# Kernel optimization log

Hardware: AMD Instinct MI355X
Metric: run time of the kernel (lower is better)

Reference implementation:

```python
import jax, jax.numpy as jnp
import numpy as np

BITS = 4            # OPU.bits
VEC = 64            # OPU.input_vector_len / weight_vector_len
QMAX = 2 ** (BITS - 1) - 1   # 7


def ste_round(x):
    # straight-through round (onn_round)
    return x + jax.lax.stop_gradient(jnp.round(x) - x)


@jax.custom_vjp
def onn_dot_sum(x, w):
    # x: [N, R, VEC], w: [VEC, R, M]
    # per-chunk matmul -> clamp to int8 range -> binarize (>=0 -> 1) -> sum over chunks
    s = jnp.einsum('nrc,crm->nrm', x, w)
    s = jnp.clip(s, -128.0, 127.0)
    return jnp.where(s < 0, 0.0, 1.0).sum(axis=1)  # [N, M]


def _onn_dot_fwd(x, w):
    return onn_dot_sum(x, w), (x, w)


def _onn_dot_bwd(res, g):
    # onn_dot_fun.backward: straight-through past clamp+threshold;
    # each chunk receives the same grad g (sum over chunks).
    x, w = res
    gx = jnp.einsum('nm,crm->nrc', g, w)
    gw = jnp.einsum('nrc,nm->crm', x, g)
    return gx, gw


onn_dot_sum.defvjp(_onn_dot_fwd, _onn_dot_bwd)


def _onn_conv2d(inp, weight):
    B, C, H, W = inp.shape
    Cout, Cin, k, _ = weight.shape
    pad = (k - 1) // 2  # SAME, stride=1
    # im2col (matches torch F.unfold channel-major ordering: C, kh, kw)
    xp = jnp.pad(inp, ((0, 0), (0, 0), (pad, pad), (pad, pad)))
    patches = jnp.stack([xp[:, :, i:i + H, j:j + W]
                         for i in range(k) for j in range(k)], axis=2)  # [B,C,k*k,H,W]
    inp_unf = patches.reshape(B, C * k * k, H * W).transpose(0, 2, 1)    # [B,L,D]
    # weight quantization: STE round + clamp to 4-bit signed range
    scale = (2 ** BITS - 1) / (weight.max() - weight.min() + 1e-9)
    wq = jnp.clip(ste_round(weight * scale), -QMAX, QMAX)
    w_ = wq.reshape(Cout, -1).T                                          # [D, Cout]
    D = C * k * k
    repeats = -(-D // VEC)
    padD = VEC * repeats - D
    x = jnp.pad(inp_unf, ((0, 0), (0, 0), (0, padD))).reshape(B * H * W, repeats, VEC)
    wpad = jnp.pad(w_, ((0, padD), (0, 0)))                              # [VEC*R, Cout]
    wr = wpad.T.reshape(Cout, repeats, VEC).transpose(2, 1, 0)           # [VEC,R,Cout]
    temp = onn_dot_sum(x, wr)                                            # [B*L, Cout]
    return temp.reshape(B, H * W, Cout).transpose(0, 2, 1).reshape(B, Cout, H, W)


def setup_inputs() -> dict:
    key = jax.random.key(0)
    k1, k2 = jax.random.split(key)
    B, Cin, H, W = 16, 128, 32, 32
    Cout, k = 256, 3
    inp = jax.random.normal(k1, (B, Cin, H, W), dtype=jnp.float32)
    fan_in = Cin * k * k
    bound = 1.0 / np.sqrt(fan_in)  # kaiming_uniform with a=sqrt(5)
    weight = jax.random.uniform(k2, (Cout, Cin, k, k), dtype=jnp.float32,
                                minval=-bound, maxval=bound)
    return {"inp": inp, "weight": weight}


def reference(inp, weight):
    return _onn_conv2d(inp, weight)
```

## Files before the change

### kernel.cpp

```cpp
#include <hip/hip_runtime.h>


#define TAU 0.03f
#define HITCAP 2048

typedef short short8 __attribute__((ext_vector_type(8)));
typedef float f32x4 __attribute__((ext_vector_type(4)));
typedef unsigned int uv4 __attribute__((ext_vector_type(4)));

__device__ __forceinline__ unsigned short bf16rn(float v) {
    unsigned u = __float_as_uint(v);
    unsigned r = u + 0x7fffu + ((u >> 16) & 1u);
    return (unsigned short)(r >> 16);
}

__global__ __launch_bounds__(256) void k_prep(const float* __restrict__ w,
                                              const float* __restrict__ inp,
                                              float* __restrict__ pmin,
                                              float* __restrict__ pmax,
                                              unsigned* __restrict__ xpk) {
    if (blockIdx.x < 64) {
        int tid = blockIdx.x * 256 + threadIdx.x;
        float vmin = 1e30f, vmax = -1e30f;
        for (int i = tid; i < 294912; i += 64 * 256) {
            float v = w[i];
            vmin = fminf(vmin, v);
            vmax = fmaxf(vmax, v);
        }
        #pragma unroll
        for (int off = 32; off > 0; off >>= 1) {
            vmin = fminf(vmin, __shfl_down(vmin, off, 64));
            vmax = fmaxf(vmax, __shfl_down(vmax, off, 64));
        }
        __shared__ float smin[4], smax[4];
        int wave = threadIdx.x >> 6;
        if ((threadIdx.x & 63) == 0) { smin[wave] = vmin; smax[wave] = vmax; }
        __syncthreads();
        if (threadIdx.x == 0) {
            #pragma unroll
            for (int i = 1; i < 4; i++) {
                vmin = fminf(vmin, smin[i]);
                vmax = fmaxf(vmax, smax[i]);
            }
            pmin[blockIdx.x] = vmin;
            pmax[blockIdx.x] = vmax;
        }
    } else {
        int bc = blockIdx.x - 64;
        const float* src = inp + (size_t)bc * 1024;
        unsigned* dst = xpk + (size_t)bc * 1156;
        #pragma unroll
        for (int i = 0; i < 5; ++i) {
            int idx = threadIdx.x + i * 256;
            if (idx < 1156) {
                int yy = idx / 34, xx = idx - yy * 34;
                float v = 0.0f;
                int ys = yy - 1, xs_ = xx - 1;
                if ((unsigned)ys < 32u && (unsigned)xs_ < 32u) v = src[ys * 32 + xs_];
                unsigned short h = bf16rn(v);
                float hf = __uint_as_float((unsigned)h << 16);
                unsigned short l = bf16rn(v - hf);
                dst[idx] = (unsigned)h | ((unsigned)l << 16);
            }
        }
    }
}

__device__ __forceinline__ float block_scale(const float* pmin, const float* pmax,
                                             float* sca_lds) {
    int t = threadIdx.x;
    if (t < 64) {
        float vmin = pmin[t];
        float vmax = pmax[t];
        #pragma unroll
        for (int off = 32; off > 0; off >>= 1) {
            vmin = fminf(vmin, __shfl_down(vmin, off, 64));
            vmax = fmaxf(vmax, __shfl_down(vmax, off, 64));
        }
        if (t == 0) {
            float tt = __fadd_rn(__fsub_rn(vmax, vmin), 1e-9f);
            *sca_lds = __fdiv_rn(15.0f, tt);
        }
    }
    __syncthreads();
    return *sca_lds;
}

__global__ __launch_bounds__(256) void k_quantb(const float* __restrict__ w,
                                                const float* __restrict__ pmin,
                                                const float* __restrict__ pmax,
                                                uv4* __restrict__ wqb) {
    __shared__ float sca;
    float s = block_scale(pmin, pmax, &sca);
    int slot = blockIdx.x * 256 + threadIdx.x;
    int lane = slot & 63;
    int sub = slot >> 6;
    int khalf = sub & 1;
    int mt = (sub >> 1) & 3;
    int gr = sub >> 3;
    int g = gr / 18, r = gr - g * 18;
    int m = g * 64 + mt * 16 + (lane & 15);
    int dbase = r * 64 + khalf * 32 + (lane >> 4) * 8;
    const float* wp = w + (size_t)m * 1152 + dbase;
    unsigned o[4];
    #pragma unroll
    for (int p = 0; p < 4; ++p) {
        float q0 = rintf(__fmul_rn(wp[2 * p], s));
        float q1 = rintf(__fmul_rn(wp[2 * p + 1], s));
        q0 = fminf(fmaxf(q0, -7.0f), 7.0f);
        q1 = fminf(fmaxf(q1, -7.0f), 7.0f);
        o[p] = (unsigned)bf16rn(q0) | ((unsigned)bf16rn(q1) << 16);
    }
    uv4 v; v.x = o[0]; v.y = o[1]; v.z = o[2]; v.w = o[3];
    wqb[slot] = v;
}

#define XLD(o) (*reinterpret_cast<const unsigned*>(xpkB + (xdelta + (unsigned)(o))))

#define ISSUE_B(rr, dst) do {                                                  \
    const int4* _oa = reinterpret_cast<const int4*>(&ofs_s[(rr) * 64 + quad * 8]); \
    int4 _o0 = _oa[0], _o1 = _oa[1];                                           \
    const int4* _ob = reinterpret_cast<const int4*>(&ofs_s[(rr) * 64 + 32 + quad * 8]); \
    int4 _o2 = _ob[0], _o3 = _ob[1];                                           \
    dst[0] = XLD(_o0.x); dst[1] = XLD(_o0.y); dst[2] = XLD(_o0.z); dst[3] = XLD(_o0.w); \
    dst[4] = XLD(_o1.x); dst[5] = XLD(_o1.y); dst[6] = XLD(_o1.z); dst[7] = XLD(_o1.w); \
    dst[8] = XLD(_o2.x); dst[9] = XLD(_o2.y); dst[10] = XLD(_o2.z); dst[11] = XLD(_o2.w); \
    dst[12] = XLD(_o3.x); dst[13] = XLD(_o3.y); dst[14] = XLD(_o3.z); dst[15] = XLD(_o3.w); \
} while (0)

#define AIDX(rr, mm) ((((mm) >> 2) * 9216) + (rr) * 512 + (((mm) & 3) * 128))

__global__ __launch_bounds__(256) void k_main(const unsigned* __restrict__ xpk,
                                              const uv4* __restrict__ wqb,
                                              const float* __restrict__ inp,
                                              const float* __restrict__ weight,
                                              const float* __restrict__ pmin,
                                              const float* __restrict__ pmax,
                                              float* __restrict__ out) {
    __shared__ alignas(16) int ofs_s[1152];
    __shared__ unsigned hitbuf[HITCAP];
    __shared__ unsigned hitcnt;
    __shared__ float sca;

    const int t = threadIdx.x;
    if (t == 0) hitcnt = 0u;
    float sc = block_scale(pmin, pmax, &sca);
    for (int k = t; k < 1152; k += 256) {
        int cin = k / 9;
        int rem = k - cin * 9;
        int kh = rem / 3;
        int kw = rem - kh * 3;
        ofs_s[k] = (cin * 1156 + kh * 34 + kw) * 4;
    }
    __syncthreads();

    const int lane = t & 63;
    const int wv = t >> 6;
    const int quad = lane >> 4;
    const int nl = lane & 15;
    const int n0 = blockIdx.x * 64;
    const int g = blockIdx.y;
    const int b = n0 >> 10;

    const int sy_w = ((n0 & 1023) >> 5) + (wv >> 1);
    const int col0 = (wv & 1) * 16;
    const char* __restrict__ xpkB = (const char*)xpk;
    const unsigned xdelta =
        ((unsigned)b * (128u * 1156u) + (unsigned)(sy_w * 34 + col0 + nl)) * 4u;
    const uv4* __restrict__ aw = wqb + (size_t)g * (2 * 18 * 512) + lane;

    unsigned negcnt[8][4] = {};
    unsigned long long hitacc = 0ull;

    unsigned pb[16];
    ISSUE_B(0, pb);
    short8 ac0 = __builtin_bit_cast(short8, aw[0]);
    short8 ac1 = __builtin_bit_cast(short8, aw[64]);

    for (int r = 0; r < 18; ++r) {
        short8 bhi[2], blo[2];
        #pragma unroll
        for (int kh2 = 0; kh2 < 2; ++kh2) {
            union { unsigned d[4]; short8 v; } H, L;
            #pragma unroll
            for (int p = 0; p < 4; ++p) {
                unsigned ua = pb[kh2 * 8 + 2 * p], ub = pb[kh2 * 8 + 2 * p + 1];
                H.d[p] = __builtin_amdgcn_perm(ub, ua, 0x05040100u);
                L.d[p] = __builtin_amdgcn_perm(ub, ua, 0x07060302u);
            }
            bhi[kh2] = H.v;
            blo[kh2] = L.v;
        }

        const int rn = (r < 17) ? r + 1 : 17;
        ISSUE_B(rn, pb);

        f32x4 accs[8];
        #pragma unroll
        for (int mt = 0; mt < 8; ++mt) {
            const int pn = (mt == 7) ? AIDX(rn, 0) : AIDX(r, mt + 1);
            short8 an0 = __builtin_bit_cast(short8, aw[pn]);
            short8 an1 = __builtin_bit_cast(short8, aw[pn + 64]);

            f32x4 acc = {0.0f, 0.0f, 0.0f, 0.0f};
            acc = __builtin_amdgcn_mfma_f32_16x16x32_bf16(ac0, bhi[0], acc, 0, 0, 0);
            acc = __builtin_amdgcn_mfma_f32_16x16x32_bf16(ac1, bhi[1], acc, 0, 0, 0);
            acc = __builtin_amdgcn_mfma_f32_16x16x32_bf16(ac0, blo[0], acc, 0, 0, 0);
            acc = __builtin_amdgcn_mfma_f32_16x16x32_bf16(ac1, blo[1], acc, 0, 0, 0);
            accs[mt] = acc;
            #pragma unroll
            for (int i = 0; i < 4; ++i) {
                negcnt[mt][i] += __float_as_uint(acc[i]) >> 31;
                hitacc |= __ballot(__builtin_fabsf(acc[i]) < TAU);
            }
            ac0 = an0;
            ac1 = an1;
        }

        if (hitacc) {
            #pragma unroll
            for (int mt = 0; mt < 8; ++mt)
                #pragma unroll
                for (int i = 0; i < 4; ++i) {
                    float s = accs[mt][i];
                    if (__builtin_fabsf(s) < TAU) {
                        unsigned ge = (__float_as_uint(s) >> 31) ^ 1u;
                        unsigned idx = atomicAdd(&hitcnt, 1u);
                        if (idx < (unsigned)HITCAP) {
                            unsigned m = (unsigned)(g * 128 + mt * 16 + quad * 4 + i);
                            unsigned n = (unsigned)(n0 + wv * 16 + nl);
                            hitbuf[idx] = n | ((unsigned)r << 14) | (m << 19)
                                            | (ge << 27);
                        }
                    }
                }
            hitacc = 0ull;
        }
    }

    {
        const int n = n0 + wv * 16 + nl;
        const int p = n & 1023;
        #pragma unroll
        for (int mt = 0; mt < 8; ++mt)
            #pragma unroll
            for (int i = 0; i < 4; ++i) {
                int m = g * 128 + mt * 16 + quad * 4 + i;
                out[(((size_t)(b * 256 + m)) << 10) + p] =
                    (float)(18u - negcnt[mt][i]);
            }
    }

    __syncthreads();
    unsigned tot = hitcnt;
    if (tot > (unsigned)HITCAP) tot = (unsigned)HITCAP;
    for (unsigned i = t; i < tot; i += 256) {
        unsigned u = hitbuf[i];
        int n = u & 16383;
        int r = (u >> 14) & 31;
        int m = (u >> 19) & 255;
        int bit = (u >> 27) & 1;
        int bb = n >> 10, p = n & 1023, y = p >> 5, x = p & 31;
        const float* ib = inp + (size_t)bb * (128 * 32 * 32);
        const float* wp = weight + (size_t)m * 1152;
        float s = 0.0f;
        int d = r * 64;
        for (int c = 0; c < 64; ++c, ++d) {
            int ci = d / 9, rem = d - ci * 9;
            int kh = rem / 3, kw = rem - kh * 3;
            int yy = y + kh - 1, xx = x + kw - 1;
            float xv = 0.0f;
            if ((unsigned)yy < 32u && (unsigned)xx < 32u)
                xv = ib[(ci * 32 + yy) * 32 + xx];
            float q = rintf(__fmul_rn(wp[d], sc));
            q = fminf(fmaxf(q, -7.0f), 7.0f);
            s = __fadd_rn(s, __fmul_rn(xv, q));
        }
        int nb = (s >= 0.0f) ? 1 : 0;
        if (nb != bit)
            atomicAdd(&out[(((size_t)(bb * 256 + m)) << 10) + p], nb ? 1.0f : -1.0f);
    }
}

extern "C" void kernel_launch(void* const* d_in, const int* in_sizes, int n_in,
                              void* d_out, int out_size, void* d_ws, size_t ws_size,
                              hipStream_t stream) {
    const float* inp    = (const float*)d_in[0];
    const float* weight = (const float*)d_in[1];
    float* out = (float*)d_out;

    char* ws = (char*)d_ws;
    float*    pmin  = (float*)(ws + 0);
    float*    pmax  = (float*)(ws + 256);
    uv4*      wqb   = (uv4*)(ws + 1024);
    unsigned* xpk   = (unsigned*)(ws + 590848);

    k_prep<<<2112, 256, 0, stream>>>(weight, inp, pmin, pmax, xpk);
    k_quantb<<<144, 256, 0, stream>>>(weight, pmin, pmax, wqb);

    dim3 grid(256, 2);
    k_main<<<grid, 256, 0, stream>>>(xpk, wqb, inp, weight, pmin, pmax, out);
}
```

Measured before the change: 124.2 us.

## Split K-chunk loop across two wave groups with shared-memory count reduction

The main kernel now runs 512 threads per block. Each pair of waves splits the 18 chunk iterations into two halves of nine, which halves the serial loop length per wave and doubles the waves per block to hide latency. Per-chunk negative counts are packed two per register to save VGPRs. The upper half writes its counts through shared memory for the lower half to sum before storing. This adds a block barrier, extra LDS and higher per-block register demand under launch_bounds(512,4).

```diff
diff --git a/kernel.cpp b/kernel.cpp
--- a/kernel.cpp
+++ b/kernel.cpp
@@ -130,22 +130,23 @@
 
 #define AIDX(rr, mm) ((((mm) >> 2) * 9216) + (rr) * 512 + (((mm) & 3) * 128))
 
-__global__ __launch_bounds__(256) void k_main(const unsigned* __restrict__ xpk,
-                                              const uv4* __restrict__ wqb,
-                                              const float* __restrict__ inp,
-                                              const float* __restrict__ weight,
-                                              const float* __restrict__ pmin,
-                                              const float* __restrict__ pmax,
-                                              float* __restrict__ out) {
+__global__ __launch_bounds__(512, 4) void k_main(const unsigned* __restrict__ xpk,
+                                                 const uv4* __restrict__ wqb,
+                                                 const float* __restrict__ inp,
+                                                 const float* __restrict__ weight,
+                                                 const float* __restrict__ pmin,
+                                                 const float* __restrict__ pmax,
+                                                 float* __restrict__ out) {
     __shared__ alignas(16) int ofs_s[1152];
     __shared__ unsigned hitbuf[HITCAP];
+    __shared__ unsigned red_s[4][64][9];
     __shared__ unsigned hitcnt;
     __shared__ float sca;
 
     const int t = threadIdx.x;
     if (t == 0) hitcnt = 0u;
     float sc = block_scale(pmin, pmax, &sca);
-    for (int k = t; k < 1152; k += 256) {
+    for (int k = t; k < 1152; k += 512) {
         int cin = k / 9;
         int rem = k - cin * 9;
         int kh = rem / 3;
@@ -155,29 +156,32 @@
     __syncthreads();
 
     const int lane = t & 63;
-    const int wv = t >> 6;
+    const int wv8 = t >> 6;
+    const int nt = wv8 >> 1;
+    const int kz = wv8 & 1;
     const int quad = lane >> 4;
     const int nl = lane & 15;
     const int n0 = blockIdx.x * 64;
     const int g = blockIdx.y;
     const int b = n0 >> 10;
-
-    const int sy_w = ((n0 & 1023) >> 5) + (wv >> 1);
-    const int col0 = (wv & 1) * 16;
+    const int r0 = kz * 9, rend = r0 + 9;
+
+    const int sy_w = ((n0 & 1023) >> 5) + (nt >> 1);
+    const int col0 = (nt & 1) * 16;
     const char* __restrict__ xpkB = (const char*)xpk;
     const unsigned xdelta =
         ((unsigned)b * (128u * 1156u) + (unsigned)(sy_w * 34 + col0 + nl)) * 4u;
     const uv4* __restrict__ aw = wqb + (size_t)g * (2 * 18 * 512) + lane;
 
-    unsigned negcnt[8][4] = {};
+    unsigned negpk[8][2] = {};
     unsigned long long hitacc = 0ull;
 
     unsigned pb[16];
-    ISSUE_B(0, pb);
-    short8 ac0 = __builtin_bit_cast(short8, aw[0]);
-    short8 ac1 = __builtin_bit_cast(short8, aw[64]);
-
-    for (int r = 0; r < 18; ++r) {
+    ISSUE_B(r0, pb);
+    short8 ac0 = __builtin_bit_cast(short8, aw[AIDX(r0, 0)]);
+    short8 ac1 = __builtin_bit_cast(short8, aw[AIDX(r0, 0) + 64]);
+
+    for (int r = r0; r < rend; ++r) {
         short8 bhi[2], blo[2];
         #pragma unroll
         for (int kh2 = 0; kh2 < 2; ++kh2) {
@@ -192,7 +196,7 @@
             blo[kh2] = L.v;
         }
 
-        const int rn = (r < 17) ? r + 1 : 17;
+        const int rn = (r + 1 < rend) ? r + 1 : r;
         ISSUE_B(rn, pb);
 
         f32x4 accs[8];
@@ -209,9 +213,12 @@
             acc = __builtin_amdgcn_mfma_f32_16x16x32_bf16(ac1, blo[1], acc, 0, 0, 0);
             accs[mt] = acc;
             #pragma unroll
-            for (int i = 0; i < 4; ++i) {
-                negcnt[mt][i] += __float_as_uint(acc[i]) >> 31;
-                hitacc |= __ballot(__builtin_fabsf(acc[i]) < TAU);
+            for (int p = 0; p < 2; ++p) {
+                unsigned sb0 = __float_as_uint(acc[2 * p]) >> 31;
+                unsigned sb1 = __float_as_uint(acc[2 * p + 1]) >> 31;
+                negpk[mt][p] += sb0 + (sb1 << 16);
+                hitacc |= __ballot(__builtin_fabsf(acc[2 * p]) < TAU);
+                hitacc |= __ballot(__builtin_fabsf(acc[2 * p + 1]) < TAU);
             }
             ac0 = an0;
             ac1 = an1;
@@ -228,7 +235,7 @@
                         unsigned idx = atomicAdd(&hitcnt, 1u);
                         if (idx < (unsigned)HITCAP) {
                             unsigned m = (unsigned)(g * 128 + mt * 16 + quad * 4 + i);
-                            unsigned n = (unsigned)(n0 + wv * 16 + nl);
+                            unsigned n = (unsigned)(n0 + nt * 16 + nl);
                             hitbuf[idx] = n | ((unsigned)r << 14) | (m << 19)
                                             | (ge << 27);
                         }
@@ -238,23 +245,38 @@
         }
     }
 
-    {
-        const int n = n0 + wv * 16 + nl;
+    if (kz == 1) {
+        #pragma unroll
+        for (int mt = 0; mt < 8; ++mt) {
+            unsigned c0 = negpk[mt][0] & 0xffffu, c1 = negpk[mt][0] >> 16;
+            unsigned c2 = negpk[mt][1] & 0xffffu, c3 = negpk[mt][1] >> 16;
+            red_s[nt][lane][mt] = c0 | (c1 << 8) | (c2 << 16) | (c3 << 24);
+        }
+    }
+    __syncthreads();
+    if (kz == 0) {
+        const int n = n0 + nt * 16 + nl;
         const int p = n & 1023;
         #pragma unroll
-        for (int mt = 0; mt < 8; ++mt)
-            #pragma unroll
-            for (int i = 0; i < 4; ++i) {
-                int m = g * 128 + mt * 16 + quad * 4 + i;
-                out[(((size_t)(b * 256 + m)) << 10) + p] =
-                    (float)(18u - negcnt[mt][i]);
-            }
+        for (int mt = 0; mt < 8; ++mt) {
+            unsigned pk = red_s[nt][lane][mt];
+            unsigned tot0 = (negpk[mt][0] & 0xffffu) + (pk & 255u);
+            unsigned tot1 = (negpk[mt][0] >> 16) + ((pk >> 8) & 255u);
+            unsigned tot2 = (negpk[mt][1] & 0xffffu) + ((pk >> 16) & 255u);
+            unsigned tot3 = (negpk[mt][1] >> 16) + (pk >> 24);
+            int mb = g * 128 + mt * 16 + quad * 4;
+            size_t obase = ((size_t)(b * 256 + mb)) << 10;
+            out[obase + p]              = (float)(18u - tot0);
+            out[obase + (1ull << 10) + p] = (float)(18u - tot1);
+            out[obase + (2ull << 10) + p] = (float)(18u - tot2);
+            out[obase + (3ull << 10) + p] = (float)(18u - tot3);
+        }
     }
 
     __syncthreads();
     unsigned tot = hitcnt;
     if (tot > (unsigned)HITCAP) tot = (unsigned)HITCAP;
-    for (unsigned i = t; i < tot; i += 256) {
+    for (unsigned i = t; i < tot; i += 512) {
         unsigned u = hitbuf[i];
         int n = u & 16383;
         int r = (u >> 14) & 31;
@@ -299,5 +321,5 @@
     k_quantb<<<144, 256, 0, stream>>>(weight, pmin, pmax, wqb);
 
     dim3 grid(256, 2);
-    k_main<<<grid, 256, 0, stream>>>(xpk, wqb, inp, weight, pmin, pmax, out);
-}
+    k_main<<<grid, 512, 0, stream>>>(xpk, wqb, inp, weight, pmin, pmax, out);
+}
```

New measurement: 119.3 us. -4.0%, faster.
